# Kernel optimization log

Hardware: AMD Instinct MI355X
Metric: run time of the kernel (lower is better)

## Reference

```python
import jax, jax.numpy as jnp
import numpy as np

N, NA, LAYERS = 8, 4, 4
NTOT = N + NA
DIM = 2 ** NTOT
B = 1024

# Diagonal of the fixed CZ brick layer (CZ is diagonal, so one elementwise pass per layer).
# Qubit 0 is the most-significant bit of the state index (tensorcircuit convention).
def _cz_diag():
    idx = np.arange(DIM)
    bits = (idx[None, :] >> (NTOT - 1 - np.arange(NTOT)[:, None])) & 1  # [NTOT, DIM]
    par = np.zeros(DIM, dtype=np.int64)
    for i in range(NTOT // 2):
        par += bits[2 * i] * bits[2 * i + 1]
    for i in range((NTOT - 1) // 2):
        par += bits[2 * i + 1] * bits[2 * i + 2]
    return jnp.asarray(1.0 - 2.0 * (par % 2), dtype=jnp.complex64)

CZ_DIAG = _cz_diag()

def _apply_1q(state, U, q):
    # state: [B, DIM]; apply 2x2 unitary U on qubit q (batched over samples)
    l, r = 2 ** q, 2 ** (NTOT - q - 1)
    s = state.reshape(-1, l, 2, r)
    return jnp.einsum('ij,bljr->blir', U, s).reshape(-1, DIM)

def _back_circuit(state, params):
    # hardware-efficient ansatz: per layer RX,RY on every qubit, then CZ bricks
    for lay in range(LAYERS):
        off = 2 * NTOT * lay
        for q in range(NTOT):
            th = params[off + q] * 0.5
            c = jnp.cos(th).astype(jnp.complex64)
            ms = (-1j) * jnp.sin(th).astype(jnp.complex64)
            Rx = jnp.stack([jnp.stack([c, ms]), jnp.stack([ms, c])])
            state = _apply_1q(state, Rx, q)
            th = params[off + NTOT + q] * 0.5
            c, s = jnp.cos(th), jnp.sin(th)
            Ry = jnp.stack([jnp.stack([c, -s]), jnp.stack([s, c])]).astype(jnp.complex64)
            state = _apply_1q(state, Ry, q)
        state = state * CZ_DIAG
    return state

def setup_inputs() -> dict:
    key = jax.random.key(0)
    k1, k2, k3, k4 = jax.random.split(key, 4)
    return {
        'inputs_re': jax.random.normal(k1, (B, DIM), jnp.float32),
        'inputs_im': jax.random.normal(k2, (B, DIM), jnp.float32),
        'params': jax.random.normal(k3, (2 * NTOT * LAYERS,), jnp.float32),
        'u': jax.random.uniform(k4, (B,), jnp.float32),
    }

def reference(inputs_re, inputs_im, params, u):
    state = (inputs_re + 1j * inputs_im).astype(jnp.complex64)
    full = _back_circuit(state, params)                      # [B, 2^n_tot]
    s3 = full.reshape(B, 2 ** NA, 2 ** N)                    # [B, 2^na, 2^n]
    probs = jnp.sum(s3.real ** 2 + s3.imag ** 2, axis=2)     # ancilla outcome probs
    cdf = jnp.cumsum(probs, axis=1)
    thresh = u * cdf[:, -1]                                  # inverse-CDF multinomial
    m = jnp.argmax(cdf >= thresh[:, None], axis=1)           # [B] sampled outcome
    post = s3[jnp.arange(B), m]                              # [B, 2^n] collapsed state
    norm = jnp.sqrt(jnp.sum(post.real ** 2 + post.imag ** 2, axis=1, keepdims=True))
    post = post / norm
    return jnp.stack([post.real, post.imag], axis=-1)        # [B, 2^n, 2]
```

## Files before the change

### kernel.cpp

```cpp
#include <hip/hip_runtime.h>
#include <math.h>

#define NTOT   12
#define DIM    4096
#define LAYERS 4
#define NB     1024
#define SPAD   4608

typedef float v2f __attribute__((ext_vector_type(2)));

template<int G>
__device__ __forceinline__ void gate_pk(v2f (&x)[16], v2f P1, v2f P2) {
#pragma unroll
    for (int p = 0; p < 8; ++p) {
        const int j0 = ((p >> G) << (G + 1)) | (p & ((1 << G) - 1));
        const int j1 = j0 | (1 << G);
        const v2f x0 = x[j0], x1 = x[j1];
        v2f t, u;
        asm("v_pk_mul_f32 %0, %1, %2 op_sel:[1,1] op_sel_hi:[1,0] neg_hi:[1,0]"
            : "=v"(t) : "v"(P2), "v"(x1));
        asm("v_pk_fma_f32 %0, %1, %2, %0 op_sel:[1,0,0] op_sel_hi:[1,1,1] neg_lo:[1,0,0] neg_hi:[1,0,0]"
            : "+v"(t) : "v"(P1), "v"(x1));
        asm("v_pk_fma_f32 %0, %1, %2, %0 op_sel:[0,1,0] op_sel_hi:[0,0,1] neg_lo:[1,0,0]"
            : "+v"(t) : "v"(P2), "v"(x0));
        asm("v_pk_fma_f32 %0, %1, %2, %0 op_sel:[0,0,0] op_sel_hi:[0,1,1]"
            : "+v"(t) : "v"(P1), "v"(x0));
        asm("v_pk_mul_f32 %0, %1, %2 op_sel:[0,1] op_sel_hi:[0,0] neg_hi:[1,0]"
            : "=v"(u) : "v"(P2), "v"(x1));
        asm("v_pk_fma_f32 %0, %1, %2, %0 op_sel:[0,0,0] op_sel_hi:[0,1,1]"
            : "+v"(u) : "v"(P1), "v"(x1));
        asm("v_pk_fma_f32 %0, %1, %2, %0 op_sel:[1,1,0] op_sel_hi:[1,0,1] neg_hi:[1,0,0]"
            : "+v"(u) : "v"(P2), "v"(x0));
        asm("v_pk_fma_f32 %0, %1, %2, %0 op_sel:[1,0,0] op_sel_hi:[1,1,1]"
            : "+v"(u) : "v"(P1), "v"(x0));
        x[j0] = t; x[j1] = u;
    }
}

__global__ __launch_bounds__(256, 4) void qddpm_kernel(
    const float* __restrict__ in_re,
    const float* __restrict__ in_im,
    const float* __restrict__ params,
    const float* __restrict__ uu,
    float* __restrict__ out)
{
    __shared__ v2f    S[SPAD];
    __shared__ float4 gco[48];
    __shared__ float  sprob[16];

    const int b = blockIdx.x;
    const int t = threadIdx.x;
    const float uval = uu[b];

    {
        const float4* re4 = (const float4*)(in_re + (size_t)b * DIM);
        const float4* im4 = (const float4*)(in_im + (size_t)b * DIM);
#pragma unroll
        for (int k = 0; k < 4; ++k) {
            const int g  = k * 256 + t;
            const float4 vr = re4[g];
            const float4 vi = im4[g];
            const int pb = g * 4 + (g >> 2) * 2;
            float4* dst = (float4*)(S + pb);
            dst[0] = make_float4(vr.x, vi.x, vr.y, vi.y);
            dst[1] = make_float4(vr.z, vi.z, vr.w, vi.w);
        }
        if (t < 48) {
            const int lay = t / 12, q = t - lay * 12;
            float c1, s1, c2, s2;
            sincosf(params[lay * 24 + q] * 0.5f, &s1, &c1);
            sincosf(params[lay * 24 + 12 + q] * 0.5f, &s2, &c2);
            gco[t] = make_float4(c1 * c2, c1 * s2, s1 * s2, s1 * c2);
        }
    }

    const int baseA = t + 2 * (t >> 4);
    const int baseB = (t >> 4) * 288 + (t & 15);
    const int baseC = t * 18;

    int sw[16];
#pragma unroll
    for (int j = 0; j < 16; ++j) {
        const int i = t * 16 + j;
        sw[j] = (__popc(i & (i >> 1) & 0x7FF) & 1) << 31;
    }

    v2f x[16];
    v2f acc2 = (v2f){0.0f, 0.0f};

    __syncthreads();

#pragma unroll 1
    for (int lay = 0; lay < LAYERS; ++lay) {
        const int gb = lay * 12;

#pragma unroll
        for (int j = 0; j < 16; ++j) x[j] = S[baseA + 288 * j];
        { float4 c;
          c = gco[gb + 3]; gate_pk<0>(x, (v2f){c.x,c.y}, (v2f){c.z,c.w});
          c = gco[gb + 2]; gate_pk<1>(x, (v2f){c.x,c.y}, (v2f){c.z,c.w});
          c = gco[gb + 1]; gate_pk<2>(x, (v2f){c.x,c.y}, (v2f){c.z,c.w});
          c = gco[gb + 0]; gate_pk<3>(x, (v2f){c.x,c.y}, (v2f){c.z,c.w}); }
#pragma unroll
        for (int j = 0; j < 16; ++j) S[baseA + 288 * j] = x[j];
        __syncthreads();

#pragma unroll
        for (int j = 0; j < 16; ++j) x[j] = S[baseB + 18 * j];
        { float4 c;
          c = gco[gb + 7]; gate_pk<0>(x, (v2f){c.x,c.y}, (v2f){c.z,c.w});
          c = gco[gb + 6]; gate_pk<1>(x, (v2f){c.x,c.y}, (v2f){c.z,c.w});
          c = gco[gb + 5]; gate_pk<2>(x, (v2f){c.x,c.y}, (v2f){c.z,c.w});
          c = gco[gb + 4]; gate_pk<3>(x, (v2f){c.x,c.y}, (v2f){c.z,c.w}); }
#pragma unroll
        for (int j = 0; j < 16; ++j) S[baseB + 18 * j] = x[j];
        __syncthreads();

        {
            const float4* src = (const float4*)(S + baseC);
#pragma unroll
            for (int q = 0; q < 4; ++q) {
                const float4 v = src[q];
                x[2 * q]     = (v2f){v.x, v.y};
                x[2 * q + 1] = (v2f){v.z, v.w};
            }
#pragma unroll
            for (int q = 4; q < 8; ++q) {
                const float4 v = src[q];
                x[2 * q]     = (v2f){v.x, v.y};
                x[2 * q + 1] = (v2f){v.z, v.w};
            }
        }
        { float4 c;
          c = gco[gb + 11]; gate_pk<0>(x, (v2f){c.x,c.y}, (v2f){c.z,c.w});
          c = gco[gb + 10]; gate_pk<1>(x, (v2f){c.x,c.y}, (v2f){c.z,c.w});
          c = gco[gb +  9]; gate_pk<2>(x, (v2f){c.x,c.y}, (v2f){c.z,c.w});
          c = gco[gb +  8]; gate_pk<3>(x, (v2f){c.x,c.y}, (v2f){c.z,c.w}); }
#pragma unroll
        for (int j = 0; j < 16; ++j) {
            x[j].x = __uint_as_float(__float_as_uint(x[j].x) ^ sw[j]);
            x[j].y = __uint_as_float(__float_as_uint(x[j].y) ^ sw[j]);
        }
        if (lay == LAYERS - 1) {
#pragma unroll
            for (int j = 0; j < 16; ++j) acc2 += x[j] * x[j];
        }
        {
            float4* dst = (float4*)(S + baseC);
#pragma unroll
            for (int q = 0; q < 8; ++q)
                dst[q] = make_float4(x[2 * q].x, x[2 * q].y, x[2 * q + 1].x, x[2 * q + 1].y);
        }
        if (lay == LAYERS - 1) {
            float partial = acc2.x + acc2.y;
#pragma unroll
            for (int o = 8; o > 0; o >>= 1)
                partial += __shfl_down(partial, o, 16);
            if ((t & 15) == 0) sprob[t >> 4] = partial;
        }
        __syncthreads();
    }

    float cdf[16];
    {
        float a = 0.0f;
#pragma unroll
        for (int i = 0; i < 16; ++i) { a += sprob[i]; cdf[i] = a; }
        const float thresh = uval * a;
        int m = 0;
#pragma unroll
        for (int i = 15; i >= 0; --i) { if (cdf[i] >= thresh) m = i; }
        const float rn = 1.0f / sqrtf(sprob[m]);
        const v2f amp = S[baseA + 288 * m];
        ((float2*)out)[(size_t)b * 256 + t] = make_float2(amp.x * rn, amp.y * rn);
    }
}

extern "C" void kernel_launch(void* const* d_in, const int* in_sizes, int n_in,
                              void* d_out, int out_size, void* d_ws, size_t ws_size,
                              hipStream_t stream) {
    const float* in_re  = (const float*)d_in[0];
    const float* in_im  = (const float*)d_in[1];
    const float* params = (const float*)d_in[2];
    const float* u      = (const float*)d_in[3];
    float* out = (float*)d_out;
    qddpm_kernel<<<NB, 256, 0, stream>>>(in_re, in_im, params, u, out);
}
```

Measured before the change: 110.8 us.

## Reorder qubit-group passes to fuse across layers and load input directly to registers

The layer loop is unrolled and the qubit-group order alternates (C,B,A then A,B,C), so adjacent layers share the same register layout and the CZ diagonal plus the next layer's gates run without a shared-memory round trip. The first group's gates are applied directly on globally loaded registers, skipping the initial staging into shared memory. This removes several LDS passes and barriers per block, at the cost of two CZ sign tables per thread and more unrolled code, which may raise register pressure.

Result: no change. 108.7 us (-1.9%).

```diff
diff --git a/kernel.cpp b/kernel.cpp
--- a/kernel.cpp
+++ b/kernel.cpp
@@ -37,6 +37,22 @@
     }
 }
 
+__device__ __forceinline__ void apply4(v2f (&x)[16], const float4* gco, int base) {
+    float4 c;
+    c = gco[base + 3]; gate_pk<0>(x, (v2f){c.x, c.y}, (v2f){c.z, c.w});
+    c = gco[base + 2]; gate_pk<1>(x, (v2f){c.x, c.y}, (v2f){c.z, c.w});
+    c = gco[base + 1]; gate_pk<2>(x, (v2f){c.x, c.y}, (v2f){c.z, c.w});
+    c = gco[base + 0]; gate_pk<3>(x, (v2f){c.x, c.y}, (v2f){c.z, c.w});
+}
+
+__device__ __forceinline__ void applyCZ(v2f (&x)[16], const int (&sw)[16]) {
+#pragma unroll
+    for (int j = 0; j < 16; ++j) {
+        x[j].x = __uint_as_float(__float_as_uint(x[j].x) ^ sw[j]);
+        x[j].y = __uint_as_float(__float_as_uint(x[j].y) ^ sw[j]);
+    }
+}
+
 __global__ __launch_bounds__(256, 4) void qddpm_kernel(
     const float* __restrict__ in_re,
     const float* __restrict__ in_im,
@@ -52,117 +68,148 @@
     const int t = threadIdx.x;
     const float uval = uu[b];
 
-    {
-        const float4* re4 = (const float4*)(in_re + (size_t)b * DIM);
-        const float4* im4 = (const float4*)(in_im + (size_t)b * DIM);
-#pragma unroll
-        for (int k = 0; k < 4; ++k) {
-            const int g  = k * 256 + t;
-            const float4 vr = re4[g];
-            const float4 vi = im4[g];
-            const int pb = g * 4 + (g >> 2) * 2;
-            float4* dst = (float4*)(S + pb);
-            dst[0] = make_float4(vr.x, vi.x, vr.y, vi.y);
-            dst[1] = make_float4(vr.z, vi.z, vr.w, vi.w);
-        }
-        if (t < 48) {
-            const int lay = t / 12, q = t - lay * 12;
-            float c1, s1, c2, s2;
-            sincosf(params[lay * 24 + q] * 0.5f, &s1, &c1);
-            sincosf(params[lay * 24 + 12 + q] * 0.5f, &s2, &c2);
-            gco[t] = make_float4(c1 * c2, c1 * s2, s1 * s2, s1 * c2);
-        }
-    }
-
     const int baseA = t + 2 * (t >> 4);
     const int baseB = (t >> 4) * 288 + (t & 15);
     const int baseC = t * 18;
 
-    int sw[16];
+    v2f x[16];
+
+    {
+        const float4* re4 = (const float4*)(in_re + (size_t)b * DIM + t * 16);
+        const float4* im4 = (const float4*)(in_im + (size_t)b * DIM + t * 16);
+#pragma unroll
+        for (int q = 0; q < 4; ++q) {
+            const float4 vr = re4[q];
+            const float4 vi = im4[q];
+            x[4 * q + 0] = (v2f){vr.x, vi.x};
+            x[4 * q + 1] = (v2f){vr.y, vi.y};
+            x[4 * q + 2] = (v2f){vr.z, vi.z};
+            x[4 * q + 3] = (v2f){vr.w, vi.w};
+        }
+    }
+    if (t < 48) {
+        const int lay = t / 12, q = t - lay * 12;
+        float c1, s1, c2, s2;
+        sincosf(params[lay * 24 + q] * 0.5f, &s1, &c1);
+        sincosf(params[lay * 24 + 12 + q] * 0.5f, &s2, &c2);
+        gco[t] = make_float4(c1 * c2, c1 * s2, s1 * s2, s1 * c2);
+    }
+
+    int swA[16], swC[16];
 #pragma unroll
     for (int j = 0; j < 16; ++j) {
-        const int i = t * 16 + j;
-        sw[j] = (__popc(i & (i >> 1) & 0x7FF) & 1) << 31;
-    }
-
-    v2f x[16];
-    v2f acc2 = (v2f){0.0f, 0.0f};
-
-    __syncthreads();
-
-#pragma unroll 1
-    for (int lay = 0; lay < LAYERS; ++lay) {
-        const int gb = lay * 12;
-
-#pragma unroll
-        for (int j = 0; j < 16; ++j) x[j] = S[baseA + 288 * j];
-        { float4 c;
-          c = gco[gb + 3]; gate_pk<0>(x, (v2f){c.x,c.y}, (v2f){c.z,c.w});
-          c = gco[gb + 2]; gate_pk<1>(x, (v2f){c.x,c.y}, (v2f){c.z,c.w});
-          c = gco[gb + 1]; gate_pk<2>(x, (v2f){c.x,c.y}, (v2f){c.z,c.w});
-          c = gco[gb + 0]; gate_pk<3>(x, (v2f){c.x,c.y}, (v2f){c.z,c.w}); }
-#pragma unroll
-        for (int j = 0; j < 16; ++j) S[baseA + 288 * j] = x[j];
-        __syncthreads();
-
-#pragma unroll
-        for (int j = 0; j < 16; ++j) x[j] = S[baseB + 18 * j];
-        { float4 c;
-          c = gco[gb + 7]; gate_pk<0>(x, (v2f){c.x,c.y}, (v2f){c.z,c.w});
-          c = gco[gb + 6]; gate_pk<1>(x, (v2f){c.x,c.y}, (v2f){c.z,c.w});
-          c = gco[gb + 5]; gate_pk<2>(x, (v2f){c.x,c.y}, (v2f){c.z,c.w});
-          c = gco[gb + 4]; gate_pk<3>(x, (v2f){c.x,c.y}, (v2f){c.z,c.w}); }
-#pragma unroll
-        for (int j = 0; j < 16; ++j) S[baseB + 18 * j] = x[j];
-        __syncthreads();
-
-        {
-            const float4* src = (const float4*)(S + baseC);
-#pragma unroll
-            for (int q = 0; q < 4; ++q) {
-                const float4 v = src[q];
-                x[2 * q]     = (v2f){v.x, v.y};
-                x[2 * q + 1] = (v2f){v.z, v.w};
-            }
-#pragma unroll
-            for (int q = 4; q < 8; ++q) {
-                const float4 v = src[q];
-                x[2 * q]     = (v2f){v.x, v.y};
-                x[2 * q + 1] = (v2f){v.z, v.w};
-            }
+        const int iC = t * 16 + j;
+        swC[j] = (__popc(iC & (iC >> 1) & 0x7FF) & 1) << 31;
+        const int iA = j * 256 + t;
+        swA[j] = (__popc(iA & (iA >> 1) & 0x7FF) & 1) << 31;
+    }
+
+    __syncthreads();
+
+    apply4(x, gco, 0 * 12 + 8);
+    {
+        float4* dst = (float4*)(S + baseC);
+#pragma unroll
+        for (int q = 0; q < 8; ++q)
+            dst[q] = make_float4(x[2 * q].x, x[2 * q].y, x[2 * q + 1].x, x[2 * q + 1].y);
+    }
+    __syncthreads();
+
+#pragma unroll
+    for (int j = 0; j < 16; ++j) x[j] = S[baseB + 18 * j];
+    apply4(x, gco, 0 * 12 + 4);
+#pragma unroll
+    for (int j = 0; j < 16; ++j) S[baseB + 18 * j] = x[j];
+    __syncthreads();
+
+#pragma unroll
+    for (int j = 0; j < 16; ++j) x[j] = S[baseA + 288 * j];
+    apply4(x, gco, 0 * 12 + 0);
+    applyCZ(x, swA);
+    apply4(x, gco, 1 * 12 + 0);
+#pragma unroll
+    for (int j = 0; j < 16; ++j) S[baseA + 288 * j] = x[j];
+    __syncthreads();
+
+#pragma unroll
+    for (int j = 0; j < 16; ++j) x[j] = S[baseB + 18 * j];
+    apply4(x, gco, 1 * 12 + 4);
+#pragma unroll
+    for (int j = 0; j < 16; ++j) S[baseB + 18 * j] = x[j];
+    __syncthreads();
+
+    {
+        const float4* src = (const float4*)(S + baseC);
+#pragma unroll
+        for (int q = 0; q < 8; ++q) {
+            const float4 v = src[q];
+            x[2 * q]     = (v2f){v.x, v.y};
+            x[2 * q + 1] = (v2f){v.z, v.w};
         }
-        { float4 c;
-          c = gco[gb + 11]; gate_pk<0>(x, (v2f){c.x,c.y}, (v2f){c.z,c.w});
-          c = gco[gb + 10]; gate_pk<1>(x, (v2f){c.x,c.y}, (v2f){c.z,c.w});
-          c = gco[gb +  9]; gate_pk<2>(x, (v2f){c.x,c.y}, (v2f){c.z,c.w});
-          c = gco[gb +  8]; gate_pk<3>(x, (v2f){c.x,c.y}, (v2f){c.z,c.w}); }
-#pragma unroll
-        for (int j = 0; j < 16; ++j) {
-            x[j].x = __uint_as_float(__float_as_uint(x[j].x) ^ sw[j]);
-            x[j].y = __uint_as_float(__float_as_uint(x[j].y) ^ sw[j]);
+    }
+    apply4(x, gco, 1 * 12 + 8);
+    applyCZ(x, swC);
+    apply4(x, gco, 2 * 12 + 8);
+    {
+        float4* dst = (float4*)(S + baseC);
+#pragma unroll
+        for (int q = 0; q < 8; ++q)
+            dst[q] = make_float4(x[2 * q].x, x[2 * q].y, x[2 * q + 1].x, x[2 * q + 1].y);
+    }
+    __syncthreads();
+
+#pragma unroll
+    for (int j = 0; j < 16; ++j) x[j] = S[baseB + 18 * j];
+    apply4(x, gco, 2 * 12 + 4);
+#pragma unroll
+    for (int j = 0; j < 16; ++j) S[baseB + 18 * j] = x[j];
+    __syncthreads();
+
+#pragma unroll
+    for (int j = 0; j < 16; ++j) x[j] = S[baseA + 288 * j];
+    apply4(x, gco, 2 * 12 + 0);
+    applyCZ(x, swA);
+    apply4(x, gco, 3 * 12 + 0);
+#pragma unroll
+    for (int j = 0; j < 16; ++j) S[baseA + 288 * j] = x[j];
+    __syncthreads();
+
+#pragma unroll
+    for (int j = 0; j < 16; ++j) x[j] = S[baseB + 18 * j];
+    apply4(x, gco, 3 * 12 + 4);
+#pragma unroll
+    for (int j = 0; j < 16; ++j) S[baseB + 18 * j] = x[j];
+    __syncthreads();
+
+    {
+        const float4* src = (const float4*)(S + baseC);
+#pragma unroll
+        for (int q = 0; q < 8; ++q) {
+            const float4 v = src[q];
+            x[2 * q]     = (v2f){v.x, v.y};
+            x[2 * q + 1] = (v2f){v.z, v.w};
         }
-        if (lay == LAYERS - 1) {
-#pragma unroll
-            for (int j = 0; j < 16; ++j) acc2 += x[j] * x[j];
-        }
-        {
-            float4* dst = (float4*)(S + baseC);
-#pragma unroll
-            for (int q = 0; q < 8; ++q)
-                dst[q] = make_float4(x[2 * q].x, x[2 * q].y, x[2 * q + 1].x, x[2 * q + 1].y);
-        }
-        if (lay == LAYERS - 1) {
-            float partial = acc2.x + acc2.y;
-#pragma unroll
-            for (int o = 8; o > 0; o >>= 1)
-                partial += __shfl_down(partial, o, 16);
-            if ((t & 15) == 0) sprob[t >> 4] = partial;
-        }
-        __syncthreads();
-    }
-
-    float cdf[16];
-    {
+    }
+    apply4(x, gco, 3 * 12 + 8);
+    applyCZ(x, swC);
+    {
+        v2f acc2 = (v2f){0.0f, 0.0f};
+#pragma unroll
+        for (int j = 0; j < 16; ++j) acc2 += x[j] * x[j];
+        float4* dst = (float4*)(S + baseC);
+#pragma unroll
+        for (int q = 0; q < 8; ++q)
+            dst[q] = make_float4(x[2 * q].x, x[2 * q].y, x[2 * q + 1].x, x[2 * q + 1].y);
+        float partial = acc2.x + acc2.y;
+#pragma unroll
+        for (int o = 8; o > 0; o >>= 1)
+            partial += __shfl_down(partial, o, 16);
+        if ((t & 15) == 0) sprob[t >> 4] = partial;
+    }
+    __syncthreads();
+
+    {
+        float cdf[16];
         float a = 0.0f;
 #pragma unroll
         for (int i = 0; i < 16; ++i) { a += sprob[i]; cdf[i] = a; }
```

## Process each sample with one wavefront holding 64 amplitudes per lane

Applied to the files above, without the earlier changes.

Restructures the kernel so each block is a single 64-lane wavefront. Each lane holds 64 complex amplitudes in registers, so a layer applies its 12 qubit rotations in two 6-qubit passes with one LDS transpose instead of three 4-qubit passes. Inputs are loaded straight from global memory into registers on the first layer. The CZ sign pattern is encoded as precomputed 64-bit masks, and block barriers are dropped because only one wave touches LDS. In exchange, register pressure is much higher and there are only a few waves per CU, which may expose memory and LDS latency. It also relies on in-order LDS access within a wave instead of explicit barriers.

Measured after the change: 116.9 us. 5.5% more time.

```diff
diff --git a/kernel.cpp b/kernel.cpp
--- a/kernel.cpp
+++ b/kernel.cpp
@@ -5,14 +5,14 @@
 #define DIM    4096
 #define LAYERS 4
 #define NB     1024
-#define SPAD   4608
+#define SPAD   4160
 
 typedef float v2f __attribute__((ext_vector_type(2)));
 
 template<int G>
-__device__ __forceinline__ void gate_pk(v2f (&x)[16], v2f P1, v2f P2) {
+__device__ __forceinline__ void gate_pk64(v2f (&x)[64], v2f P1, v2f P2) {
 #pragma unroll
-    for (int p = 0; p < 8; ++p) {
+    for (int p = 0; p < 32; ++p) {
         const int j0 = ((p >> G) << (G + 1)) | (p & ((1 << G) - 1));
         const int j1 = j0 | (1 << G);
         const v2f x0 = x[j0], x1 = x[j1];
@@ -37,7 +37,29 @@
     }
 }
 
-__global__ __launch_bounds__(256, 4) void qddpm_kernel(
+__device__ __forceinline__ void apply6(v2f (&x)[64], const float4* gco, int top) {
+    float4 c;
+    c = gco[top - 0]; gate_pk64<0>(x, (v2f){c.x, c.y}, (v2f){c.z, c.w});
+    c = gco[top - 1]; gate_pk64<1>(x, (v2f){c.x, c.y}, (v2f){c.z, c.w});
+    c = gco[top - 2]; gate_pk64<2>(x, (v2f){c.x, c.y}, (v2f){c.z, c.w});
+    c = gco[top - 3]; gate_pk64<3>(x, (v2f){c.x, c.y}, (v2f){c.z, c.w});
+    c = gco[top - 4]; gate_pk64<4>(x, (v2f){c.x, c.y}, (v2f){c.z, c.w});
+    c = gco[top - 5]; gate_pk64<5>(x, (v2f){c.x, c.y}, (v2f){c.z, c.w});
+}
+
+__device__ __forceinline__ void applyCZ64(v2f (&x)[64], unsigned long long mask) {
+#pragma unroll
+    for (int j = 0; j < 64; ++j) {
+        const unsigned int w = (j < 32) ? (unsigned int)mask : (unsigned int)(mask >> 32);
+        const unsigned int sw = (w << (31 - (j & 31))) & 0x80000000u;
+        x[j].x = __uint_as_float(__float_as_uint(x[j].x) ^ sw);
+        x[j].y = __uint_as_float(__float_as_uint(x[j].y) ^ sw);
+    }
+}
+
+#define KPAR 0xB8B7B8484748B848ULL
+
+__global__ __launch_bounds__(64, 1) void qddpm_kernel(
     const float* __restrict__ in_re,
     const float* __restrict__ in_im,
     const float* __restrict__ params,
@@ -49,120 +71,64 @@
     __shared__ float  sprob[16];
 
     const int b = blockIdx.x;
-    const int t = threadIdx.x;
+    const int l = threadIdx.x;
     const float uval = uu[b];
 
-    {
-        const float4* re4 = (const float4*)(in_re + (size_t)b * DIM);
-        const float4* im4 = (const float4*)(in_im + (size_t)b * DIM);
-#pragma unroll
-        for (int k = 0; k < 4; ++k) {
-            const int g  = k * 256 + t;
-            const float4 vr = re4[g];
-            const float4 vi = im4[g];
-            const int pb = g * 4 + (g >> 2) * 2;
-            float4* dst = (float4*)(S + pb);
-            dst[0] = make_float4(vr.x, vi.x, vr.y, vi.y);
-            dst[1] = make_float4(vr.z, vi.z, vr.w, vi.w);
-        }
-        if (t < 48) {
-            const int lay = t / 12, q = t - lay * 12;
-            float c1, s1, c2, s2;
-            sincosf(params[lay * 24 + q] * 0.5f, &s1, &c1);
-            sincosf(params[lay * 24 + 12 + q] * 0.5f, &s2, &c2);
-            gco[t] = make_float4(c1 * c2, c1 * s2, s1 * s2, s1 * c2);
-        }
+    if (l < 48) {
+        const int lay = l / 12, q = l - lay * 12;
+        float c1, s1, c2, s2;
+        sincosf(params[lay * 24 + q] * 0.5f, &s1, &c1);
+        sincosf(params[lay * 24 + 12 + q] * 0.5f, &s2, &c2);
+        gco[l] = make_float4(c1 * c2, c1 * s2, s1 * s2, s1 * c2);
     }
 
-    const int baseA = t + 2 * (t >> 4);
-    const int baseB = (t >> 4) * 288 + (t & 15);
-    const int baseC = t * 18;
+    const unsigned long long parl = ((KPAR >> l) & 1ULL) ? ~0ULL : 0ULL;
+    const unsigned long long maskQ =
+        KPAR ^ parl ^ ((l & 1)  ? 0xFFFFFFFF00000000ULL : 0ULL);
+    const unsigned long long maskP =
+        KPAR ^ parl ^ ((l & 32) ? 0xAAAAAAAAAAAAAAAAULL : 0ULL);
 
-    int sw[16];
-#pragma unroll
-    for (int j = 0; j < 16; ++j) {
-        const int i = t * 16 + j;
-        sw[j] = (__popc(i & (i >> 1) & 0x7FF) & 1) << 31;
-    }
-
-    v2f x[16];
+    v2f x[64];
     v2f acc2 = (v2f){0.0f, 0.0f};
-
-    __syncthreads();
 
 #pragma unroll 1
     for (int lay = 0; lay < LAYERS; ++lay) {
-        const int gb = lay * 12;
+        if (lay == 0) {
+            const float* re = in_re + (size_t)b * DIM + l;
+            const float* im = in_im + (size_t)b * DIM + l;
+#pragma unroll
+            for (int j = 0; j < 64; ++j)
+                x[j] = (v2f){re[64 * j], im[64 * j]};
+        } else {
+#pragma unroll
+            for (int j = 0; j < 64; ++j) x[j] = S[65 * j + l];
+        }
+        apply6(x, gco, lay * 12 + 5);
+#pragma unroll
+        for (int j = 0; j < 64; ++j) S[65 * j + l] = x[j];
 
 #pragma unroll
-        for (int j = 0; j < 16; ++j) x[j] = S[baseA + 288 * j];
-        { float4 c;
-          c = gco[gb + 3]; gate_pk<0>(x, (v2f){c.x,c.y}, (v2f){c.z,c.w});
-          c = gco[gb + 2]; gate_pk<1>(x, (v2f){c.x,c.y}, (v2f){c.z,c.w});
-          c = gco[gb + 1]; gate_pk<2>(x, (v2f){c.x,c.y}, (v2f){c.z,c.w});
-          c = gco[gb + 0]; gate_pk<3>(x, (v2f){c.x,c.y}, (v2f){c.z,c.w}); }
-#pragma unroll
-        for (int j = 0; j < 16; ++j) S[baseA + 288 * j] = x[j];
-        __syncthreads();
-
-#pragma unroll
-        for (int j = 0; j < 16; ++j) x[j] = S[baseB + 18 * j];
-        { float4 c;
-          c = gco[gb + 7]; gate_pk<0>(x, (v2f){c.x,c.y}, (v2f){c.z,c.w});
-          c = gco[gb + 6]; gate_pk<1>(x, (v2f){c.x,c.y}, (v2f){c.z,c.w});
-          c = gco[gb + 5]; gate_pk<2>(x, (v2f){c.x,c.y}, (v2f){c.z,c.w});
-          c = gco[gb + 4]; gate_pk<3>(x, (v2f){c.x,c.y}, (v2f){c.z,c.w}); }
-#pragma unroll
-        for (int j = 0; j < 16; ++j) S[baseB + 18 * j] = x[j];
-        __syncthreads();
-
-        {
-            const float4* src = (const float4*)(S + baseC);
-#pragma unroll
-            for (int q = 0; q < 4; ++q) {
-                const float4 v = src[q];
-                x[2 * q]     = (v2f){v.x, v.y};
-                x[2 * q + 1] = (v2f){v.z, v.w};
-            }
-#pragma unroll
-            for (int q = 4; q < 8; ++q) {
-                const float4 v = src[q];
-                x[2 * q]     = (v2f){v.x, v.y};
-                x[2 * q + 1] = (v2f){v.z, v.w};
-            }
-        }
-        { float4 c;
-          c = gco[gb + 11]; gate_pk<0>(x, (v2f){c.x,c.y}, (v2f){c.z,c.w});
-          c = gco[gb + 10]; gate_pk<1>(x, (v2f){c.x,c.y}, (v2f){c.z,c.w});
-          c = gco[gb +  9]; gate_pk<2>(x, (v2f){c.x,c.y}, (v2f){c.z,c.w});
-          c = gco[gb +  8]; gate_pk<3>(x, (v2f){c.x,c.y}, (v2f){c.z,c.w}); }
-#pragma unroll
-        for (int j = 0; j < 16; ++j) {
-            x[j].x = __uint_as_float(__float_as_uint(x[j].x) ^ sw[j]);
-            x[j].y = __uint_as_float(__float_as_uint(x[j].y) ^ sw[j]);
-        }
+        for (int j = 0; j < 64; ++j) x[j] = S[65 * l + j];
+        apply6(x, gco, lay * 12 + 11);
+        applyCZ64(x, maskQ);
         if (lay == LAYERS - 1) {
 #pragma unroll
-            for (int j = 0; j < 16; ++j) acc2 += x[j] * x[j];
+            for (int j = 0; j < 64; ++j) acc2 += x[j] * x[j];
         }
-        {
-            float4* dst = (float4*)(S + baseC);
 #pragma unroll
-            for (int q = 0; q < 8; ++q)
-                dst[q] = make_float4(x[2 * q].x, x[2 * q].y, x[2 * q + 1].x, x[2 * q + 1].y);
-        }
-        if (lay == LAYERS - 1) {
-            float partial = acc2.x + acc2.y;
-#pragma unroll
-            for (int o = 8; o > 0; o >>= 1)
-                partial += __shfl_down(partial, o, 16);
-            if ((t & 15) == 0) sprob[t >> 4] = partial;
-        }
-        __syncthreads();
+        for (int j = 0; j < 64; ++j) S[65 * l + j] = x[j];
+    }
+    (void)maskP;
+
+    {
+        float partial = acc2.x + acc2.y;
+        partial += __shfl_down(partial, 2, 4);
+        partial += __shfl_down(partial, 1, 4);
+        if ((l & 3) == 0) sprob[l >> 2] = partial;
     }
 
-    float cdf[16];
     {
+        float cdf[16];
         float a = 0.0f;
 #pragma unroll
         for (int i = 0; i < 16; ++i) { a += sprob[i]; cdf[i] = a; }
@@ -171,8 +137,13 @@
 #pragma unroll
         for (int i = 15; i >= 0; --i) { if (cdf[i] >= thresh) m = i; }
         const float rn = 1.0f / sqrtf(sprob[m]);
-        const v2f amp = S[baseA + 288 * m];
-        ((float2*)out)[(size_t)b * 256 + t] = make_float2(amp.x * rn, amp.y * rn);
+
+        float2* o2 = (float2*)out + (size_t)b * 256;
+#pragma unroll
+        for (int c = 0; c < 4; ++c) {
+            const v2f amp = S[260 * m + 65 * c + l];
+            o2[c * 64 + l] = make_float2(amp.x * rn, amp.y * rn);
+        }
     }
 }
 
@@ -184,5 +155,5 @@
     const float* params = (const float*)d_in[2];
     const float* u      = (const float*)d_in[3];
     float* out = (float*)d_out;
-    qddpm_kernel<<<NB, 256, 0, stream>>>(in_re, in_im, params, u, out);
+    qddpm_kernel<<<NB, 64, 0, stream>>>(in_re, in_im, params, u, out);
 }
```

## Keep state in registers, apply gates via cross-lane DPP/swizzle and fused 2-qubit LDS exchange

Applied to the files above, without the earlier changes.

Each thread now loads its 16 contiguous amplitudes straight from global memory into registers instead of staging them through shared memory. Per layer, the two top qubits (wave-crossing bits) are applied together as a fused 4x4 complex combination read from LDS partners. The six mid qubits use intra-wave DPP, ds_swizzle and bpermute exchanges, and the four low qubits stay in-register. This cuts the three LDS round trips and transposes per layer down to one store/load exchange, with fewer barriers. The cost is more cross-lane instructions and sign-selection logic, and possible precision drift from the fused gate coefficients.

After: 118.5 us. 6.9% more time.

```diff
diff --git a/kernel.cpp b/kernel.cpp
--- a/kernel.cpp
+++ b/kernel.cpp
@@ -1,13 +1,19 @@
 #include <hip/hip_runtime.h>
 #include <math.h>
 
-#define NTOT   12
 #define DIM    4096
 #define LAYERS 4
 #define NB     1024
-#define SPAD   4608
+#define SSLOT  17
 
 typedef float v2f __attribute__((ext_vector_type(2)));
+
+__device__ __forceinline__ v2f cmul(v2f a, v2f b) {
+    return (v2f){a.x * b.x - a.y * b.y, a.x * b.y + a.y * b.x};
+}
+__device__ __forceinline__ float fxor(float f, unsigned m) {
+    return __uint_as_float(__float_as_uint(f) ^ m);
+}
 
 template<int G>
 __device__ __forceinline__ void gate_pk(v2f (&x)[16], v2f P1, v2f P2) {
@@ -37,6 +43,50 @@
     }
 }
 
+template<typename F>
+__device__ __forceinline__ void gate_lane(v2f (&x)[16], v2f P1, v2f P2, F fetch) {
+#pragma unroll
+    for (int j = 0; j < 16; ++j) {
+        v2f p;
+        p.x = fetch(x[j].x);
+        p.y = fetch(x[j].y);
+        v2f t;
+        asm("v_pk_mul_f32 %0, %1, %2 op_sel:[1,1] op_sel_hi:[1,0] neg_hi:[1,0]"
+            : "=v"(t) : "v"(P2), "v"(p));
+        asm("v_pk_fma_f32 %0, %1, %2, %0 op_sel:[1,0,0] op_sel_hi:[1,1,1]"
+            : "+v"(t) : "v"(P1), "v"(p));
+        asm("v_pk_fma_f32 %0, %1, %2, %0 op_sel:[0,1,0] op_sel_hi:[0,0,1] neg_lo:[1,0,0]"
+            : "+v"(t) : "v"(P2), "v"(x[j]));
+        asm("v_pk_fma_f32 %0, %1, %2, %0 op_sel:[0,0,0] op_sel_hi:[0,1,1]"
+            : "+v"(t) : "v"(P1), "v"(x[j]));
+        x[j] = t;
+    }
+}
+
+__device__ __forceinline__ v2f cmac_init(v2f M, v2f v) {
+    v2f acc;
+    asm("v_pk_mul_f32 %0, %1, %2 op_sel:[0,0] op_sel_hi:[0,1]"
+        : "=v"(acc) : "v"(M), "v"(v));
+    asm("v_pk_fma_f32 %0, %1, %2, %0 op_sel:[1,1,0] op_sel_hi:[1,0,1] neg_lo:[1,0,0]"
+        : "+v"(acc) : "v"(M), "v"(v));
+    return acc;
+}
+__device__ __forceinline__ void cmac(v2f& acc, v2f M, v2f v) {
+    asm("v_pk_fma_f32 %0, %1, %2, %0 op_sel:[0,0,0] op_sel_hi:[0,1,1]"
+        : "+v"(acc) : "v"(M), "v"(v));
+    asm("v_pk_fma_f32 %0, %1, %2, %0 op_sel:[1,1,0] op_sel_hi:[1,0,1] neg_lo:[1,0,0]"
+        : "+v"(acc) : "v"(M), "v"(v));
+}
+
+struct FDpp1 { __device__ float operator()(float f) const {
+    return __int_as_float(__builtin_amdgcn_update_dpp(0, __float_as_int(f), 0xB1, 0xF, 0xF, false)); } };
+struct FDpp2 { __device__ float operator()(float f) const {
+    return __int_as_float(__builtin_amdgcn_update_dpp(0, __float_as_int(f), 0x4E, 0xF, 0xF, false)); } };
+template<int IMM> struct FSwz { __device__ float operator()(float f) const {
+    return __int_as_float(__builtin_amdgcn_ds_swizzle(__float_as_int(f), IMM)); } };
+struct FBp { int a; __device__ float operator()(float f) const {
+    return __int_as_float(__builtin_amdgcn_ds_bpermute(a, __float_as_int(f))); } };
+
 __global__ __launch_bounds__(256, 4) void qddpm_kernel(
     const float* __restrict__ in_re,
     const float* __restrict__ in_im,
@@ -44,125 +94,119 @@
     const float* __restrict__ uu,
     float* __restrict__ out)
 {
-    __shared__ v2f    S[SPAD];
+    __shared__ v2f    S[256 * SSLOT];
     __shared__ float4 gco[48];
     __shared__ float  sprob[16];
 
     const int b = blockIdx.x;
     const int t = threadIdx.x;
+    const int l = t & 63;
     const float uval = uu[b];
 
+    v2f x[16];
     {
-        const float4* re4 = (const float4*)(in_re + (size_t)b * DIM);
-        const float4* im4 = (const float4*)(in_im + (size_t)b * DIM);
-#pragma unroll
-        for (int k = 0; k < 4; ++k) {
-            const int g  = k * 256 + t;
-            const float4 vr = re4[g];
-            const float4 vi = im4[g];
-            const int pb = g * 4 + (g >> 2) * 2;
-            float4* dst = (float4*)(S + pb);
-            dst[0] = make_float4(vr.x, vi.x, vr.y, vi.y);
-            dst[1] = make_float4(vr.z, vi.z, vr.w, vi.w);
+        const float4* re4 = (const float4*)(in_re + (size_t)b * DIM + t * 16);
+        const float4* im4 = (const float4*)(in_im + (size_t)b * DIM + t * 16);
+#pragma unroll
+        for (int q = 0; q < 4; ++q) {
+            const float4 vr = re4[q];
+            const float4 vi = im4[q];
+            x[4 * q + 0] = (v2f){vr.x, vi.x};
+            x[4 * q + 1] = (v2f){vr.y, vi.y};
+            x[4 * q + 2] = (v2f){vr.z, vi.z};
+            x[4 * q + 3] = (v2f){vr.w, vi.w};
         }
-        if (t < 48) {
-            const int lay = t / 12, q = t - lay * 12;
-            float c1, s1, c2, s2;
-            sincosf(params[lay * 24 + q] * 0.5f, &s1, &c1);
-            sincosf(params[lay * 24 + 12 + q] * 0.5f, &s2, &c2);
-            gco[t] = make_float4(c1 * c2, c1 * s2, s1 * s2, s1 * c2);
-        }
-    }
-
-    const int baseA = t + 2 * (t >> 4);
-    const int baseB = (t >> 4) * 288 + (t & 15);
-    const int baseC = t * 18;
-
-    int sw[16];
+    }
+    if (l < 48) {
+        const int lay = l / 12, q = l - lay * 12;
+        float c1, s1, c2, s2;
+        sincosf(params[lay * 24 + q] * 0.5f, &s1, &c1);
+        sincosf(params[lay * 24 + 12 + q] * 0.5f, &s2, &c2);
+        gco[l] = make_float4(c1 * c2, c1 * s2, s1 * s2, s1 * c2);
+    }
+    int smask = 0;
 #pragma unroll
     for (int j = 0; j < 16; ++j) {
         const int i = t * 16 + j;
-        sw[j] = (__popc(i & (i >> 1) & 0x7FF) & 1) << 31;
-    }
-
-    v2f x[16];
-    v2f acc2 = (v2f){0.0f, 0.0f};
-
-    __syncthreads();
+        smask |= (__popc(i & (i >> 1) & 0x7FF) & 1) << j;
+    }
+    const int sbase = t * SSLOT;
+    const int bp32  = (l ^ 32) << 2;
 
 #pragma unroll 1
     for (int lay = 0; lay < LAYERS; ++lay) {
         const int gb = lay * 12;
 
-#pragma unroll
-        for (int j = 0; j < 16; ++j) x[j] = S[baseA + 288 * j];
-        { float4 c;
-          c = gco[gb + 3]; gate_pk<0>(x, (v2f){c.x,c.y}, (v2f){c.z,c.w});
-          c = gco[gb + 2]; gate_pk<1>(x, (v2f){c.x,c.y}, (v2f){c.z,c.w});
-          c = gco[gb + 1]; gate_pk<2>(x, (v2f){c.x,c.y}, (v2f){c.z,c.w});
-          c = gco[gb + 0]; gate_pk<3>(x, (v2f){c.x,c.y}, (v2f){c.z,c.w}); }
-#pragma unroll
-        for (int j = 0; j < 16; ++j) S[baseA + 288 * j] = x[j];
+        if (lay) __syncthreads();
+#pragma unroll
+        for (int r = 0; r < 16; ++r) S[sbase + r] = x[r];
         __syncthreads();
-
-#pragma unroll
-        for (int j = 0; j < 16; ++j) x[j] = S[baseB + 18 * j];
-        { float4 c;
-          c = gco[gb + 7]; gate_pk<0>(x, (v2f){c.x,c.y}, (v2f){c.z,c.w});
-          c = gco[gb + 6]; gate_pk<1>(x, (v2f){c.x,c.y}, (v2f){c.z,c.w});
-          c = gco[gb + 5]; gate_pk<2>(x, (v2f){c.x,c.y}, (v2f){c.z,c.w});
-          c = gco[gb + 4]; gate_pk<3>(x, (v2f){c.x,c.y}, (v2f){c.z,c.w}); }
-#pragma unroll
-        for (int j = 0; j < 16; ++j) S[baseB + 18 * j] = x[j];
-        __syncthreads();
-
         {
-            const float4* src = (const float4*)(S + baseC);
-#pragma unroll
-            for (int q = 0; q < 4; ++q) {
-                const float4 v = src[q];
-                x[2 * q]     = (v2f){v.x, v.y};
-                x[2 * q + 1] = (v2f){v.z, v.w};
-            }
-#pragma unroll
-            for (int q = 4; q < 8; ++q) {
-                const float4 v = src[q];
-                x[2 * q]     = (v2f){v.x, v.y};
-                x[2 * q + 1] = (v2f){v.z, v.w};
+            const float4 g0 = gco[gb + 0], g1 = gco[gb + 1];
+            const int i0 = (t >> 7) & 1, i1 = (t >> 6) & 1;
+            const v2f ea = (v2f){g0.x, i0 ? -g0.z : g0.z};
+            const v2f eb = (v2f){i0 ? g0.y : -g0.y, -g0.w};
+            const v2f fa = (v2f){g1.x, i1 ? -g1.z : g1.z};
+            const v2f fb = (v2f){i1 ? g1.y : -g1.y, -g1.w};
+            const v2f Mo = cmul(ea, fa);
+            const v2f M1 = cmul(ea, fb);
+            const v2f M2 = cmul(eb, fa);
+            const v2f M3 = cmul(eb, fb);
+            const int p1 = (t ^ 64) * SSLOT, p2 = (t ^ 128) * SSLOT, p3 = (t ^ 192) * SSLOT;
+#pragma unroll
+            for (int r = 0; r < 16; ++r) {
+                const v2f q1 = S[p1 + r], q2 = S[p2 + r], q3 = S[p3 + r];
+                v2f acc = cmac_init(Mo, x[r]);
+                cmac(acc, M1, q1);
+                cmac(acc, M2, q2);
+                cmac(acc, M3, q3);
+                x[r] = acc;
             }
         }
-        { float4 c;
-          c = gco[gb + 11]; gate_pk<0>(x, (v2f){c.x,c.y}, (v2f){c.z,c.w});
-          c = gco[gb + 10]; gate_pk<1>(x, (v2f){c.x,c.y}, (v2f){c.z,c.w});
-          c = gco[gb +  9]; gate_pk<2>(x, (v2f){c.x,c.y}, (v2f){c.z,c.w});
-          c = gco[gb +  8]; gate_pk<3>(x, (v2f){c.x,c.y}, (v2f){c.z,c.w}); }
-#pragma unroll
-        for (int j = 0; j < 16; ++j) {
-            x[j].x = __uint_as_float(__float_as_uint(x[j].x) ^ sw[j]);
-            x[j].y = __uint_as_float(__float_as_uint(x[j].y) ^ sw[j]);
+
+        { const float4 c = gco[gb + 7]; const unsigned n = (unsigned)(l & 1) << 31;
+          gate_lane(x, (v2f){c.x, fxor(c.y, n ^ 0x80000000u)}, (v2f){fxor(c.z, n), c.w}, FDpp1{}); }
+        { const float4 c = gco[gb + 6]; const unsigned n = (unsigned)((l >> 1) & 1) << 31;
+          gate_lane(x, (v2f){c.x, fxor(c.y, n ^ 0x80000000u)}, (v2f){fxor(c.z, n), c.w}, FDpp2{}); }
+        { const float4 c = gco[gb + 5]; const unsigned n = (unsigned)((l >> 2) & 1) << 31;
+          gate_lane(x, (v2f){c.x, fxor(c.y, n ^ 0x80000000u)}, (v2f){fxor(c.z, n), c.w}, FSwz<0x101F>{}); }
+        { const float4 c = gco[gb + 4]; const unsigned n = (unsigned)((l >> 3) & 1) << 31;
+          gate_lane(x, (v2f){c.x, fxor(c.y, n ^ 0x80000000u)}, (v2f){fxor(c.z, n), c.w}, FSwz<0x201F>{}); }
+        { const float4 c = gco[gb + 3]; const unsigned n = (unsigned)((l >> 4) & 1) << 31;
+          gate_lane(x, (v2f){c.x, fxor(c.y, n ^ 0x80000000u)}, (v2f){fxor(c.z, n), c.w}, FSwz<0x401F>{}); }
+        { const float4 c = gco[gb + 2]; const unsigned n = (unsigned)((l >> 5) & 1) << 31;
+          gate_lane(x, (v2f){c.x, fxor(c.y, n ^ 0x80000000u)}, (v2f){fxor(c.z, n), c.w}, FBp{bp32}); }
+
+        { const float4 c = gco[gb + 11]; gate_pk<0>(x, (v2f){c.x, c.y}, (v2f){c.z, c.w}); }
+        { const float4 c = gco[gb + 10]; gate_pk<1>(x, (v2f){c.x, c.y}, (v2f){c.z, c.w}); }
+        { const float4 c = gco[gb +  9]; gate_pk<2>(x, (v2f){c.x, c.y}, (v2f){c.z, c.w}); }
+        { const float4 c = gco[gb +  8]; gate_pk<3>(x, (v2f){c.x, c.y}, (v2f){c.z, c.w}); }
+
+#pragma unroll
+        for (int r = 0; r < 16; ++r) {
+            const unsigned sg = (unsigned)((smask >> r) & 1) << 31;
+            x[r].x = fxor(x[r].x, sg);
+            x[r].y = fxor(x[r].y, sg);
         }
-        if (lay == LAYERS - 1) {
-#pragma unroll
-            for (int j = 0; j < 16; ++j) acc2 += x[j] * x[j];
-        }
-        {
-            float4* dst = (float4*)(S + baseC);
-#pragma unroll
-            for (int q = 0; q < 8; ++q)
-                dst[q] = make_float4(x[2 * q].x, x[2 * q].y, x[2 * q + 1].x, x[2 * q + 1].y);
-        }
-        if (lay == LAYERS - 1) {
-            float partial = acc2.x + acc2.y;
-#pragma unroll
-            for (int o = 8; o > 0; o >>= 1)
-                partial += __shfl_down(partial, o, 16);
-            if ((t & 15) == 0) sprob[t >> 4] = partial;
-        }
-        __syncthreads();
-    }
-
-    float cdf[16];
+    }
+
+    __syncthreads();
+#pragma unroll
+    for (int r = 0; r < 16; ++r) S[sbase + r] = x[r];
     {
+        v2f acc2 = (v2f){0.0f, 0.0f};
+#pragma unroll
+        for (int r = 0; r < 16; ++r) acc2 += x[r] * x[r];
+        float partial = acc2.x + acc2.y;
+#pragma unroll
+        for (int o = 8; o > 0; o >>= 1)
+            partial += __shfl_down(partial, o, 16);
+        if ((t & 15) == 0) sprob[t >> 4] = partial;
+    }
+    __syncthreads();
+
+    {
+        float cdf[16];
         float a = 0.0f;
 #pragma unroll
         for (int i = 0; i < 16; ++i) { a += sprob[i]; cdf[i] = a; }
@@ -171,7 +215,7 @@
 #pragma unroll
         for (int i = 15; i >= 0; --i) { if (cdf[i] >= thresh) m = i; }
         const float rn = 1.0f / sqrtf(sprob[m]);
-        const v2f amp = S[baseA + 288 * m];
+        const v2f amp = S[272 * m + SSLOT * (t >> 4) + (t & 15)];
         ((float2*)out)[(size_t)b * 256 + t] = make_float2(amp.x * rn, amp.y * rn);
     }
 }
```
